# Optimization experiments

Measured on AMD Instinct MI355X. Metric: run time of the kernel, lower is better.

Reference implementation:

```python
import jax, jax.numpy as jnp
import numpy as np

N, L, D = 8192, 50, 64          # batch nodes, history length, embed_dim
NUM_ITEMS, NUM_ATTRS, NUM_FAM = 50000, 100000, 100000


def setup_inputs() -> dict:
    key = jax.random.key(0)
    ks = jax.random.split(key, 12)
    scale = 0.05
    return {
        "nodes": jax.random.randint(ks[0], (N,), 0, NUM_ITEMS),
        "history_va": jax.random.randint(ks[1], (N, L), 0, NUM_ATTRS),
        "history_af": jax.random.randint(ks[2], (N, L), 0, NUM_FAM),
        "v2e_w": jax.random.normal(ks[3], (NUM_ITEMS, D), jnp.float32) * scale,
        "a2e_w": jax.random.normal(ks[4], (NUM_ATTRS, D), jnp.float32) * scale,
        "f2e_w": jax.random.normal(ks[5], (NUM_FAM, D), jnp.float32) * scale,
        "W1": jax.random.normal(ks[6], (3 * D, D), jnp.float32) * scale,
        "b1": jnp.zeros((D,), jnp.float32),
        "W2": jax.random.normal(ks[7], (D, D), jnp.float32) * scale,
        "b2": jnp.zeros((D,), jnp.float32),
        "w3": jax.random.normal(ks[8], (D, 1), jnp.float32) * scale,
        "b3": jnp.zeros((1,), jnp.float32),
    }


def reference(nodes, history_va, history_af, v2e_w, a2e_w, f2e_w,
              W1, b1, W2, b2, w3, b3):
    # Batched form of the per-node loop (va=True branch).
    e_va = a2e_w[history_va]                       # [N, L, D] gathered attr embeds
    e_af = f2e_w[history_af]                       # [N, L, D] gathered famous embeds
    va_rep = v2e_w[nodes]                          # [N, D]    target item embed
    rep = jnp.broadcast_to(va_rep[:, None, :], e_va.shape)
    x = jnp.concatenate([e_va, rep, e_af], axis=-1)  # [N, L, 3D]
    h = jax.nn.relu(x @ W1 + b1)                   # [N, L, D]
    h = jax.nn.relu(h @ W2 + b2)                   # [N, L, D]
    scores = (h @ w3 + b3)[..., 0]                 # [N, L]
    att = jax.nn.softmax(scores, axis=1)           # softmax over history dim
    # e_va.T @ att per node  ==  weighted sum over history
    return jnp.einsum("nld,nl->nd", e_va, att)     # [N, D]
```

## Files before the change

### kernel.cpp

```cpp
#include <hip/hip_runtime.h>
#include <hip/hip_bf16.h>

typedef __bf16    bf16x8 __attribute__((ext_vector_type(8)));
typedef __bf16    bf16x4 __attribute__((ext_vector_type(4)));
typedef _Float16  f16x8  __attribute__((ext_vector_type(8)));
typedef _Float16  f16x4  __attribute__((ext_vector_type(4)));
typedef float     f32x4  __attribute__((ext_vector_type(4)));

#define HL 50
#define DD 64


__global__ __launch_bounds__(256, 4) void prep_all_kernel(
    const int*   __restrict__ nodes,
    const float* __restrict__ v2e,
    const float* __restrict__ a2e,
    const float* __restrict__ f2e,
    const float* __restrict__ W1,
    const float* __restrict__ b1,
    const float* __restrict__ W2,
    const float* __restrict__ b2,
    const float* __restrict__ w3,
    _Float16* __restrict__ A2, _Float16* __restrict__ F2,
    _Float16* __restrict__ E16, _Float16* __restrict__ ba16,
    _Float16* __restrict__ w2f, float* __restrict__ wsc,
    int nA, int nF, int N, int GA, int GF, int GB)
{
    __shared__ __align__(16) _Float16 es[64 * 72];
    const int tid  = threadIdx.x;
    const int w    = tid >> 6, lane = tid & 63;
    const int lq   = lane & 15, quad = lane >> 4;
    const int col  = w * 16 + lq;
    const int bid  = blockIdx.x;

    if (bid < GA + GF) {
        const bool  isA   = (bid < GA);
        const int   rb    = isA ? bid : bid - GA;
        const int   nrows = isA ? nA : nF;
        const float* src  = isA ? a2e : f2e;
        const float* Wp   = isA ? W1 : (W1 + 128 * DD);
        _Float16*   dst   = isA ? A2 : F2;
        const int   r0    = rb * 64;

        #pragma unroll
        for (int i = 0; i < 4; ++i) {
            int t = i * 256 + tid;
            int row = t >> 4, q = t & 15;
            int gr = r0 + row; if (gr >= nrows) gr = nrows - 1;
            float4 v = *(const float4*)(src + (size_t)gr * DD + q * 4);
            f16x4 pk = {(_Float16)v.x, (_Float16)v.y, (_Float16)v.z, (_Float16)v.w};
            *(f16x4*)&es[row * 72 + q * 4] = pk;
            if (isA) *(f16x4*)(E16 + (size_t)gr * DD + q * 4) = pk;
        }
        f16x8 bfr[2];
        #pragma unroll
        for (int t = 0; t < 2; ++t)
            #pragma unroll
            for (int j = 0; j < 8; ++j)
                bfr[t][j] = (_Float16)Wp[(t * 32 + quad * 8 + j) * DD + col];
        __syncthreads();

        f32x4 acc[4];
        #pragma unroll
        for (int mt = 0; mt < 4; ++mt) acc[mt] = (f32x4){0.f, 0.f, 0.f, 0.f};
        #pragma unroll
        for (int t = 0; t < 2; ++t)
            #pragma unroll
            for (int mt = 0; mt < 4; ++mt) {
                f16x8 a = *(const f16x8*)&es[(mt * 16 + lq) * 72 + t * 32 + quad * 8];
                acc[mt] = __builtin_amdgcn_mfma_f32_16x16x32_f16(a, bfr[t], acc[mt], 0, 0, 0);
            }
        __syncthreads();
        #pragma unroll
        for (int mt = 0; mt < 4; ++mt)
            #pragma unroll
            for (int r = 0; r < 4; ++r)
                es[(mt * 16 + quad * 4 + r) * 72 + col] = (_Float16)acc[mt][r];
        __syncthreads();
        {
            #pragma unroll
            for (int h = 0; h < 2; ++h) {
                int t   = h * 256 + tid;
                int row = t >> 3, seg = t & 7;
                int gr  = r0 + row;
                if (gr < nrows) {
                    f16x8 vv = *(const f16x8*)&es[row * 72 + seg * 8];
                    *(f16x8*)(dst + (size_t)gr * DD + seg * 8) = vv;
                }
            }
        }
    } else if (bid < GA + GF + GB) {
        const int n0 = (bid - GA - GF) * 64;
        #pragma unroll
        for (int i = 0; i < 4; ++i) {
            int t = i * 256 + tid;
            int row = t >> 4, q = t & 15;
            int gn = n0 + row; if (gn >= N) gn = N - 1;
            int idx = nodes[gn];
            float4 v = *(const float4*)(v2e + (size_t)idx * DD + q * 4);
            f16x4 pk = {(_Float16)v.x, (_Float16)v.y, (_Float16)v.z, (_Float16)v.w};
            *(f16x4*)&es[row * 72 + q * 4] = pk;
        }
        f16x8 bfr[2];
        #pragma unroll
        for (int t = 0; t < 2; ++t)
            #pragma unroll
            for (int j = 0; j < 8; ++j)
                bfr[t][j] = (_Float16)W1[(64 + t * 32 + quad * 8 + j) * DD + col];
        const float b1c = b1[col];
        __syncthreads();

        f32x4 acc[4];
        #pragma unroll
        for (int mt = 0; mt < 4; ++mt) acc[mt] = (f32x4){0.f, 0.f, 0.f, 0.f};
        #pragma unroll
        for (int t = 0; t < 2; ++t)
            #pragma unroll
            for (int mt = 0; mt < 4; ++mt) {
                f16x8 a = *(const f16x8*)&es[(mt * 16 + lq) * 72 + t * 32 + quad * 8];
                acc[mt] = __builtin_amdgcn_mfma_f32_16x16x32_f16(a, bfr[t], acc[mt], 0, 0, 0);
            }
        #pragma unroll
        for (int mt = 0; mt < 4; ++mt)
            #pragma unroll
            for (int r = 0; r < 4; ++r) {
                int gn = n0 + mt * 16 + quad * 4 + r;
                if (gn < N) ba16[(size_t)gn * DD + col] = (_Float16)(acc[mt][r] + b1c);
            }
    } else {
        const int ln = tid & 63, c0 = tid >> 6;
        #pragma unroll
        for (int h = 0; h < 2; ++h) {
            int combo = c0 + 4 * h;
            int ct = combo >> 1, t = combo & 1;
            _Float16* d = w2f + ((size_t)combo * 64 + ln) * 8;
            #pragma unroll
            for (int j = 0; j < 8; ++j)
                d[j] = (_Float16)W2[(t * 32 + (ln >> 4) * 8 + j) * DD + ct * 16 + (ln & 15)];
        }
        if (tid < 64) { wsc[tid] = w3[tid]; wsc[64 + tid] = b2[tid]; }
    }
}

__global__ __launch_bounds__(256, 4) void va_main_kernel(
    const int*      __restrict__ hva,
    const int*      __restrict__ haf,
    const _Float16* __restrict__ A2,
    const _Float16* __restrict__ F2,
    const _Float16* __restrict__ E16,
    const _Float16* __restrict__ ba16,
    const _Float16* __restrict__ w2f,
    const float*    __restrict__ wsc,
    float*          __restrict__ out, int Ntot)
{
    const int tid  = threadIdx.x;
    const int w    = tid >> 6;
    const int lane = tid & 63;
    const int lq   = lane & 15;
    const int quad = lane >> 4;
    const int node = blockIdx.x * 4 + w;
    if (node >= Ntot) return;

    const int* hb = hva + node * HL;
    const int* fb = haf + node * HL;
    const int lclamp = (lane < HL) ? lane : 0;
    const int iv  = hb[lclamp];
    const int ifv = fb[lclamp];

    f16x8 bag[2];
    #pragma unroll
    for (int t = 0; t < 2; ++t)
        bag[t] = *(const f16x8*)(ba16 + (size_t)node * DD + t * 32 + quad * 8);

    f16x8 a2g[4][2], f2g[4][2];
    #pragma unroll
    for (int mt = 0; mt < 4; ++mt) {
        const int row = mt * 16 + lq;
        const int ia  = __shfl(iv,  row);
        const int ifm = __shfl(ifv, row);
        const bool valid = (row < HL);
        #pragma unroll
        for (int t = 0; t < 2; ++t) {
            if (valid) {
                a2g[mt][t] = *(const f16x8*)(A2 + (size_t)ia  * DD + t * 32 + quad * 8);
                f2g[mt][t] = *(const f16x8*)(F2 + (size_t)ifm * DD + t * 32 + quad * 8);
            }
        }
    }

    f16x8 h1f[4][2];
    #pragma unroll
    for (int mt = 0; mt < 4; ++mt) {
        const bool valid = (mt * 16 + lq) < HL;
        #pragma unroll
        for (int t = 0; t < 2; ++t) {
            f16x8 h = a2g[mt][t] + f2g[mt][t] + bag[t];
            #pragma unroll
            for (int j = 0; j < 8; ++j)
                h1f[mt][t][j] = (valid && h[j] > (_Float16)0.f) ? h[j] : (_Float16)0.f;
        }
    }

    float sc[4][4];
    #pragma unroll
    for (int mt = 0; mt < 4; ++mt)
        #pragma unroll
        for (int r = 0; r < 4; ++r) sc[mt][r] = 0.f;

    #pragma unroll
    for (int ct = 0; ct < 4; ++ct) {
        const float b2c = wsc[64 + ct * 16 + lq];
        const float w3c = wsc[ct * 16 + lq];
        f16x8 bfr[2];
        #pragma unroll
        for (int t = 0; t < 2; ++t)
            bfr[t] = *(const f16x8*)(w2f + ((size_t)(ct * 2 + t) * 64 + lane) * 8);
        #pragma unroll
        for (int mt = 0; mt < 4; ++mt) {
            f32x4 acc = {b2c, b2c, b2c, b2c};
            #pragma unroll
            for (int t = 0; t < 2; ++t)
                acc = __builtin_amdgcn_mfma_f32_16x16x32_f16(h1f[mt][t], bfr[t], acc, 0, 0, 0);
            #pragma unroll
            for (int r = 0; r < 4; ++r)
                sc[mt][r] = fmaf(fmaxf(acc[r], 0.f), w3c, sc[mt][r]);
        }
    }

    #pragma unroll
    for (int mt = 0; mt < 4; ++mt)
        #pragma unroll
        for (int r = 0; r < 4; ++r)
            #pragma unroll
            for (int m = 1; m < 16; m <<= 1)
                sc[mt][r] += __shfl_xor(sc[mt][r], m);

    #pragma unroll
    for (int r = 0; r < 4; ++r)
        if (48 + quad * 4 + r >= HL) sc[3][r] = -3.0e38f;

    float mx = sc[0][0];
    #pragma unroll
    for (int mt = 0; mt < 4; ++mt)
        #pragma unroll
        for (int r = 0; r < 4; ++r) mx = fmaxf(mx, sc[mt][r]);
    mx = fmaxf(mx, __shfl_xor(mx, 16));
    mx = fmaxf(mx, __shfl_xor(mx, 32));

    float sm = 0.f;
    #pragma unroll
    for (int mt = 0; mt < 4; ++mt)
        #pragma unroll
        for (int r = 0; r < 4; ++r) {
            sc[mt][r] = __expf(sc[mt][r] - mx);
            sm += sc[mt][r];
        }
    sm += __shfl_xor(sm, 16);
    sm += __shfl_xor(sm, 32);
    const float inv = 1.f / sm;

    float oa[4] = {0.f, 0.f, 0.f, 0.f};
    #pragma unroll
    for (int l = 0; l < HL; ++l) {
        const int   srcl = ((l >> 2) & 3) << 4;
        const float av   = __shfl(sc[l >> 4][l & 3], srcl);
        const int   idx  = __builtin_amdgcn_readlane(iv, l);
        oa[l & 3] = fmaf(av, (float)E16[(size_t)idx * DD + lane], oa[l & 3]);
    }
    out[(size_t)node * DD + lane] = ((oa[0] + oa[1]) + (oa[2] + oa[3])) * inv;
}

#define FMR  112
#define FMT  7
#define FXSS 136

__global__ __launch_bounds__(256) void fb_prep_kernel(
    const float* __restrict__ W1, const float* __restrict__ W2,
    const float* __restrict__ w3, const float* __restrict__ b1,
    const float* __restrict__ b2,
    __bf16* __restrict__ wf, float* __restrict__ wsc)
{
    const int tid  = threadIdx.x;
    const int quad = tid >> 6;
    const int col  = tid & 63;
    __bf16* dst = wf + tid * 64;
    #pragma unroll
    for (int t = 0; t < 4; ++t)
        #pragma unroll
        for (int j = 0; j < 8; ++j) {
            int keff = t * 32 + quad * 8 + j;
            int krow = (keff < 64) ? keff : keff + 64;
            dst[t * 8 + j] = (__bf16)W1[krow * 64 + col];
        }
    #pragma unroll
    for (int t = 0; t < 2; ++t)
        #pragma unroll
        for (int j = 0; j < 8; ++j) {
            dst[32 + t * 8 + j] = (__bf16)W1[(64 + t * 32 + quad * 8 + j) * 64 + col];
            dst[48 + t * 8 + j] = (__bf16)W2[(t * 32 + quad * 8 + j) * 64 + col];
        }
    if (tid < 64) {
        wsc[tid] = w3[tid]; wsc[64 + tid] = b1[tid]; wsc[128 + tid] = b2[tid];
    }
}

__global__ __launch_bounds__(256, 5) void fb_agg_kernel(
    const int* __restrict__ nodes, const int* __restrict__ hva,
    const int* __restrict__ haf, const float* __restrict__ v2e,
    const float* __restrict__ a2e, const float* __restrict__ f2e,
    const __bf16* __restrict__ wf, const float* __restrict__ wsc,
    float* __restrict__ out)
{
    __shared__ __bf16 xs[FMR * FXSS];
    __shared__ float  pbuf[4 * FMR];
    const int tid = threadIdx.x;
    const int w = tid >> 6, lane = tid & 63, lq = lane & 15, quad = lane >> 4;
    const int col = w * 16 + lq;
    const int n0 = blockIdx.x * 2;
    {
        const int* hb = hva + n0 * HL;
        const int* fb = haf + n0 * HL;
        #pragma unroll
        for (int i = 0; i < 13; ++i) {
            int t = i * 256 + tid;
            if (t < 2 * HL * 2 * 16) {
                int r = t >> 4, q = t & 15;
                bool va = (r < 2 * HL);
                int gr = va ? r : r - 2 * HL;
                int idx = va ? hb[gr] : fb[gr];
                const float* src = (va ? a2e : f2e) + (size_t)idx * DD + q * 4;
                float4 v = *(const float4*)src;
                bf16x4 pk = {(__bf16)v.x, (__bf16)v.y, (__bf16)v.z, (__bf16)v.w};
                *(bf16x4*)&xs[gr * FXSS + (va ? 0 : DD) + q * 4] = pk;
            }
        }
    }
    bf16x8 repf[2];
    #pragma unroll
    for (int t = 0; t < 2; ++t)
        #pragma unroll
        for (int j = 0; j < 8; ++j) repf[t][j] = (__bf16)0.f;
    if (lq < 2) {
        int nd = nodes[n0 + lq];
        const float* rp = v2e + (size_t)nd * DD;
        #pragma unroll
        for (int t = 0; t < 2; ++t) {
            float4 v0 = *(const float4*)(rp + t * 32 + quad * 8);
            float4 v1 = *(const float4*)(rp + t * 32 + quad * 8 + 4);
            repf[t] = (bf16x8){(__bf16)v0.x, (__bf16)v0.y, (__bf16)v0.z, (__bf16)v0.w,
                               (__bf16)v1.x, (__bf16)v1.y, (__bf16)v1.z, (__bf16)v1.w};
        }
    }
    const __bf16* fbp = wf + (size_t)(quad * 64 + col) * 64;
    bf16x8 b1f[4], b1u[2], b2f[2];
    #pragma unroll
    for (int t = 0; t < 4; ++t) b1f[t] = *(const bf16x8*)(fbp + t * 8);
    #pragma unroll
    for (int t = 0; t < 2; ++t) {
        b1u[t] = *(const bf16x8*)(fbp + 32 + t * 8);
        b2f[t] = *(const bf16x8*)(fbp + 48 + t * 8);
    }
    const float w3c = wsc[col];
    const float b1c = wsc[64 + col];
    const float b2c = wsc[128 + col];
    f32x4 rb = {0.f, 0.f, 0.f, 0.f};
    #pragma unroll
    for (int t = 0; t < 2; ++t)
        rb = __builtin_amdgcn_mfma_f32_16x16x32_bf16(repf[t], b1u[t], rb, 0, 0, 0);
    const float bias0 = __shfl(rb[0], lq) + b1c;
    const float bias1 = __shfl(rb[1], lq) + b1c;
    __syncthreads();
    f32x4 acc[FMT];
    #pragma unroll
    for (int mt = 0; mt < FMT; ++mt)
        #pragma unroll
        for (int r = 0; r < 4; ++r) {
            int gr = mt * 16 + quad * 4 + r;
            acc[mt][r] = (gr >= HL) ? bias1 : bias0;
        }
    #pragma unroll
    for (int t = 0; t < 4; ++t)
        #pragma unroll
        for (int mt = 0; mt < FMT; ++mt) {
            bf16x8 a = *(const bf16x8*)&xs[(mt * 16 + lq) * FXSS + t * 32 + quad * 8];
            acc[mt] = __builtin_amdgcn_mfma_f32_16x16x32_bf16(a, b1f[t], acc[mt], 0, 0, 0);
        }
    __syncthreads();
    #pragma unroll
    for (int mt = 0; mt < FMT; ++mt)
        #pragma unroll
        for (int r = 0; r < 4; ++r) {
            int gr = mt * 16 + quad * 4 + r;
            xs[gr * FXSS + DD + col] = (__bf16)fmaxf(acc[mt][r], 0.f);
        }
    __syncthreads();
    f32x4 a2[FMT];
    #pragma unroll
    for (int mt = 0; mt < FMT; ++mt) a2[mt] = (f32x4){b2c, b2c, b2c, b2c};
    #pragma unroll
    for (int t = 0; t < 2; ++t)
        #pragma unroll
        for (int mt = 0; mt < FMT; ++mt) {
            bf16x8 a = *(const bf16x8*)&xs[(mt * 16 + lq) * FXSS + DD + t * 32 + quad * 8];
            a2[mt] = __builtin_amdgcn_mfma_f32_16x16x32_bf16(a, b2f[t], a2[mt], 0, 0, 0);
        }
    #pragma unroll
    for (int mt = 0; mt < FMT; ++mt) {
        float p0 = fmaxf(a2[mt][0], 0.f) * w3c;
        float p1 = fmaxf(a2[mt][1], 0.f) * w3c;
        float p2 = fmaxf(a2[mt][2], 0.f) * w3c;
        float p3 = fmaxf(a2[mt][3], 0.f) * w3c;
        #pragma unroll
        for (int m = 1; m < 16; m <<= 1) {
            p0 += __shfl_xor(p0, m); p1 += __shfl_xor(p1, m);
            p2 += __shfl_xor(p2, m); p3 += __shfl_xor(p3, m);
        }
        if (lq == 0) {
            int rowb = mt * 16 + quad * 4;
            pbuf[w * FMR + rowb + 0] = p0; pbuf[w * FMR + rowb + 1] = p1;
            pbuf[w * FMR + rowb + 2] = p2; pbuf[w * FMR + rowb + 3] = p3;
        }
    }
    __syncthreads();
    const int n = w & 1, lh = w >> 1;
    float att;
    {
        float s = -3.0e38f;
        if (lane < HL) {
            int gr = n * HL + lane;
            s = pbuf[gr] + pbuf[FMR + gr] + pbuf[2 * FMR + gr] + pbuf[3 * FMR + gr];
        }
        float mx = s;
        #pragma unroll
        for (int m = 1; m < 64; m <<= 1) mx = fmaxf(mx, __shfl_xor(mx, m));
        float e = (lane < HL) ? __expf(s - mx) : 0.f;
        float sm = e;
        #pragma unroll
        for (int m = 1; m < 64; m <<= 1) sm += __shfl_xor(sm, m);
        att = e / sm;
    }
    {
        float o = 0.f;
        const int lb = lh * 25;
        #pragma unroll
        for (int i = 0; i < 25; ++i) {
            int l = lb + i;
            float av = __shfl(att, l);
            o = fmaf(av, (float)xs[(n * HL + l) * FXSS + lane], o);
        }
        float* op = (float*)&xs[(100 + w) * FXSS + DD];
        op[lane] = o;
    }
    __syncthreads();
    if (w < 2) {
        const float* p0 = (const float*)&xs[(100 + w) * FXSS + DD];
        const float* p1 = (const float*)&xs[(100 + w + 2) * FXSS + DD];
        out[(size_t)(n0 + w) * DD + lane] = p0[lane] + p1[lane];
    }
}

extern "C" void kernel_launch(void* const* d_in, const int* in_sizes, int n_in,
                              void* d_out, int out_size, void* d_ws, size_t ws_size,
                              hipStream_t stream) {
    const int*   nodes = (const int*)d_in[0];
    const int*   hva   = (const int*)d_in[1];
    const int*   haf   = (const int*)d_in[2];
    const float* v2e   = (const float*)d_in[3];
    const float* a2e   = (const float*)d_in[4];
    const float* f2e   = (const float*)d_in[5];
    const float* W1    = (const float*)d_in[6];
    const float* b1    = (const float*)d_in[7];
    const float* W2    = (const float*)d_in[8];
    const float* b2    = (const float*)d_in[9];
    const float* w3    = (const float*)d_in[10];
    float* out = (float*)d_out;

    const int N  = in_sizes[0];
    const int nA = in_sizes[4] / DD;
    const int nF = in_sizes[5] / DD;

    size_t offA2 = 0;
    size_t offF2 = (offA2 + (size_t)nA * DD * 2 + 255) & ~(size_t)255;
    size_t offE  = (offF2 + (size_t)nF * DD * 2 + 255) & ~(size_t)255;
    size_t offBA = (offE  + (size_t)nA * DD * 2 + 255) & ~(size_t)255;
    size_t offWF = (offBA + (size_t)N * DD * 2 + 255) & ~(size_t)255;
    size_t offSC = offWF + 8 * 64 * 8 * 2;
    size_t need  = offSC + 128 * 4;

    if (ws_size >= need) {
        _Float16* A2  = (_Float16*)((char*)d_ws + offA2);
        _Float16* F2  = (_Float16*)((char*)d_ws + offF2);
        _Float16* E16 = (_Float16*)((char*)d_ws + offE);
        _Float16* ba  = (_Float16*)((char*)d_ws + offBA);
        _Float16* w2f = (_Float16*)((char*)d_ws + offWF);
        float*    wsc = (float*)((char*)d_ws + offSC);

        const int GA = (nA + 63) / 64;
        const int GF = (nF + 63) / 64;
        const int GB = (N + 63) / 64;
        prep_all_kernel<<<GA + GF + GB + 1, 256, 0, stream>>>(
            nodes, v2e, a2e, f2e, W1, b1, W2, b2, w3,
            A2, F2, E16, ba, w2f, wsc, nA, nF, N, GA, GF, GB);
        va_main_kernel<<<(N + 3) / 4, 256, 0, stream>>>(
            hva, haf, A2, F2, E16, ba, w2f, wsc, out, N);
    } else {
        __bf16* wf  = (__bf16*)d_ws;
        float*  wsc = (float*)((char*)d_ws + 256 * 64 * 2);
        fb_prep_kernel<<<1, 256, 0, stream>>>(W1, W2, w3, b1, b2, wf, wsc);
        fb_agg_kernel<<<N / 2, 256, 0, stream>>>(nodes, hva, haf, v2e, a2e, f2e,
                                                 wf, wsc, out);
    }
}
```

Measured before the change: 149.4 us.

## Restage prep GEMM per-wave with shared weight tile and prefetch history embeds early

In the prep kernel, each wave now owns a 16-row slice and computes all 64 output columns from a weight tile staged once in shared memory. This removes two block-wide barriers, and the global loads of the input rows are issued before the weight conversion. In the main kernel, the 50 E16 history-embedding gathers for the final weighted sum are hoisted to before the MLP. Their latency can then overlap the MFMA and softmax work instead of stalling inside the last loop. The cost is higher register pressure (25 packed half2 values per lane) and more shared memory in the prep kernel, which may reduce occupancy.

```diff
diff --git a/kernel.cpp b/kernel.cpp
--- a/kernel.cpp
+++ b/kernel.cpp
@@ -5,6 +5,7 @@
 typedef __bf16    bf16x4 __attribute__((ext_vector_type(4)));
 typedef _Float16  f16x8  __attribute__((ext_vector_type(8)));
 typedef _Float16  f16x4  __attribute__((ext_vector_type(4)));
+typedef _Float16  f16x2  __attribute__((ext_vector_type(2)));
 typedef float     f32x4  __attribute__((ext_vector_type(4)));
 
 #define HL 50
@@ -26,11 +27,11 @@
     _Float16* __restrict__ w2f, float* __restrict__ wsc,
     int nA, int nF, int N, int GA, int GF, int GB)
 {
+    __shared__ __align__(16) _Float16 wlds[8 * 512];
     __shared__ __align__(16) _Float16 es[64 * 72];
     const int tid  = threadIdx.x;
     const int w    = tid >> 6, lane = tid & 63;
     const int lq   = lane & 15, quad = lane >> 4;
-    const int col  = w * 16 + lq;
     const int bid  = blockIdx.x;
 
     if (bid < GA + GF) {
@@ -40,56 +41,75 @@
         const float* src  = isA ? a2e : f2e;
         const float* Wp   = isA ? W1 : (W1 + 128 * DD);
         _Float16*   dst   = isA ? A2 : F2;
-        const int   r0    = rb * 64;
-
+        const int   r0w   = rb * 64 + w * 16;
+        _Float16*   ws_   = &es[w * 16 * 72];
+
+        float4 v[4];
+        int    grv[4];
         #pragma unroll
         for (int i = 0; i < 4; ++i) {
-            int t = i * 256 + tid;
-            int row = t >> 4, q = t & 15;
-            int gr = r0 + row; if (gr >= nrows) gr = nrows - 1;
-            float4 v = *(const float4*)(src + (size_t)gr * DD + q * 4);
-            f16x4 pk = {(_Float16)v.x, (_Float16)v.y, (_Float16)v.z, (_Float16)v.w};
-            *(f16x4*)&es[row * 72 + q * 4] = pk;
-            if (isA) *(f16x4*)(E16 + (size_t)gr * DD + q * 4) = pk;
-        }
-        f16x8 bfr[2];
+            int t = i * 64 + lane;
+            int row = t >> 4, chunk = t & 15;
+            int gr = r0w + row; if (gr >= nrows) gr = nrows - 1;
+            grv[i] = gr;
+            v[i] = *(const float4*)(src + (size_t)gr * DD + chunk * 4);
+        }
+
+        #pragma unroll
+        for (int h = 0; h < 2; ++h) {
+            int combo = w + 4 * h;
+            int ct = combo >> 1, t = combo & 1;
+            f16x8 pk;
+            #pragma unroll
+            for (int j = 0; j < 8; ++j)
+                pk[j] = (_Float16)Wp[(t * 32 + quad * 8 + j) * DD + ct * 16 + lq];
+            *(f16x8*)&wlds[(size_t)combo * 512 + lane * 8] = pk;
+        }
+
+        #pragma unroll
+        for (int i = 0; i < 4; ++i) {
+            int t = i * 64 + lane;
+            int row = t >> 4, chunk = t & 15;
+            f16x4 pk = {(_Float16)v[i].x, (_Float16)v[i].y,
+                        (_Float16)v[i].z, (_Float16)v[i].w};
+            *(f16x4*)&ws_[row * 72 + chunk * 4] = pk;
+            if (isA) *(f16x4*)(E16 + (size_t)grv[i] * DD + chunk * 4) = pk;
+        }
+
+        __syncthreads();
+
+        f16x8 afr[2];
         #pragma unroll
         for (int t = 0; t < 2; ++t)
-            #pragma unroll
-            for (int j = 0; j < 8; ++j)
-                bfr[t][j] = (_Float16)Wp[(t * 32 + quad * 8 + j) * DD + col];
-        __syncthreads();
-
+            afr[t] = *(const f16x8*)&ws_[lq * 72 + t * 32 + quad * 8];
         f32x4 acc[4];
         #pragma unroll
-        for (int mt = 0; mt < 4; ++mt) acc[mt] = (f32x4){0.f, 0.f, 0.f, 0.f};
-        #pragma unroll
-        for (int t = 0; t < 2; ++t)
-            #pragma unroll
-            for (int mt = 0; mt < 4; ++mt) {
-                f16x8 a = *(const f16x8*)&es[(mt * 16 + lq) * 72 + t * 32 + quad * 8];
-                acc[mt] = __builtin_amdgcn_mfma_f32_16x16x32_f16(a, bfr[t], acc[mt], 0, 0, 0);
+        for (int ct = 0; ct < 4; ++ct) {
+            acc[ct] = (f32x4){0.f, 0.f, 0.f, 0.f};
+            #pragma unroll
+            for (int t = 0; t < 2; ++t) {
+                f16x8 bfr = *(const f16x8*)&wlds[(size_t)(ct * 2 + t) * 512 + lane * 8];
+                acc[ct] = __builtin_amdgcn_mfma_f32_16x16x32_f16(afr[t], bfr, acc[ct], 0, 0, 0);
             }
-        __syncthreads();
-        #pragma unroll
-        for (int mt = 0; mt < 4; ++mt)
+        }
+
+        #pragma unroll
+        for (int ct = 0; ct < 4; ++ct)
             #pragma unroll
             for (int r = 0; r < 4; ++r)
-                es[(mt * 16 + quad * 4 + r) * 72 + col] = (_Float16)acc[mt][r];
-        __syncthreads();
+                ws_[(quad * 4 + r) * 72 + ct * 16 + lq] = (_Float16)acc[ct][r];
         {
-            #pragma unroll
-            for (int h = 0; h < 2; ++h) {
-                int t   = h * 256 + tid;
-                int row = t >> 3, seg = t & 7;
-                int gr  = r0 + row;
-                if (gr < nrows) {
-                    f16x8 vv = *(const f16x8*)&es[row * 72 + seg * 8];
-                    *(f16x8*)(dst + (size_t)gr * DD + seg * 8) = vv;
-                }
+            int row = lane >> 2, g = lane & 3;
+            int gr  = r0w + row;
+            if (gr < nrows) {
+                f16x8 v0 = *(const f16x8*)&ws_[row * 72 + g * 16];
+                f16x8 v1 = *(const f16x8*)&ws_[row * 72 + g * 16 + 8];
+                *(f16x8*)(dst + (size_t)gr * DD + g * 16)     = v0;
+                *(f16x8*)(dst + (size_t)gr * DD + g * 16 + 8) = v1;
             }
         }
     } else if (bid < GA + GF + GB) {
+        const int col = w * 16 + lq;
         const int n0 = (bid - GA - GF) * 64;
         #pragma unroll
         for (int i = 0; i < 4; ++i) {
@@ -188,6 +208,15 @@
         }
     }
 
+    f16x2 ev[25];
+    #pragma unroll
+    for (int i = 0; i < 25; ++i) {
+        const int i0 = __builtin_amdgcn_readlane(iv, 2 * i);
+        const int i1 = __builtin_amdgcn_readlane(iv, 2 * i + 1);
+        ev[i][0] = E16[(size_t)i0 * DD + lane];
+        ev[i][1] = E16[(size_t)i1 * DD + lane];
+    }
+
     f16x8 h1f[4][2];
     #pragma unroll
     for (int mt = 0; mt < 4; ++mt) {
@@ -264,8 +293,7 @@
     for (int l = 0; l < HL; ++l) {
         const int   srcl = ((l >> 2) & 3) << 4;
         const float av   = __shfl(sc[l >> 4][l & 3], srcl);
-        const int   idx  = __builtin_amdgcn_readlane(iv, l);
-        oa[l & 3] = fmaf(av, (float)E16[(size_t)idx * DD + lane], oa[l & 3]);
+        oa[l & 3] = fmaf(av, (float)ev[l >> 1][l & 1], oa[l & 3]);
     }
     out[(size_t)node * DD + lane] = ((oa[0] + oa[1]) + (oa[2] + oa[3])) * inv;
 }
```

Result: slower. 157.4 us (+5.4%).

## Gather raw fp32 embeddings and compute first MLP layer per node

Applied to the files above, without the earlier changes.

Stops precomputing the first-layer projections (A·W1a, F·W1f) over the entire 100k-row attribute and famous tables. The main kernel now gathers the fp32 rows for each node's history, converts them to fp16 and runs the W1 MFMAs itself, with the node bias as the accumulator init. The hidden layer goes through per-wave shared memory to be re-laid out for the W2 MFMA. This removes a full pass over both tables in the prep kernel and the fp16 copy E16. In exchange the gathers read twice the bytes (fp32), there is more compute per node, and the occupancy hint drops to 2 blocks because of register and LDS pressure.

```diff
diff --git a/kernel.cpp b/kernel.cpp
--- a/kernel.cpp
+++ b/kernel.cpp
@@ -14,83 +14,24 @@
 __global__ __launch_bounds__(256, 4) void prep_all_kernel(
     const int*   __restrict__ nodes,
     const float* __restrict__ v2e,
-    const float* __restrict__ a2e,
-    const float* __restrict__ f2e,
     const float* __restrict__ W1,
     const float* __restrict__ b1,
     const float* __restrict__ W2,
     const float* __restrict__ b2,
     const float* __restrict__ w3,
-    _Float16* __restrict__ A2, _Float16* __restrict__ F2,
-    _Float16* __restrict__ E16, _Float16* __restrict__ ba16,
-    _Float16* __restrict__ w2f, float* __restrict__ wsc,
-    int nA, int nF, int N, int GA, int GF, int GB)
+    _Float16* __restrict__ ba16,
+    _Float16* __restrict__ wf, float* __restrict__ wsc,
+    int N, int GB)
 {
     __shared__ __align__(16) _Float16 es[64 * 72];
     const int tid  = threadIdx.x;
     const int w    = tid >> 6, lane = tid & 63;
     const int lq   = lane & 15, quad = lane >> 4;
-    const int col  = w * 16 + lq;
     const int bid  = blockIdx.x;
 
-    if (bid < GA + GF) {
-        const bool  isA   = (bid < GA);
-        const int   rb    = isA ? bid : bid - GA;
-        const int   nrows = isA ? nA : nF;
-        const float* src  = isA ? a2e : f2e;
-        const float* Wp   = isA ? W1 : (W1 + 128 * DD);
-        _Float16*   dst   = isA ? A2 : F2;
-        const int   r0    = rb * 64;
-
-        #pragma unroll
-        for (int i = 0; i < 4; ++i) {
-            int t = i * 256 + tid;
-            int row = t >> 4, q = t & 15;
-            int gr = r0 + row; if (gr >= nrows) gr = nrows - 1;
-            float4 v = *(const float4*)(src + (size_t)gr * DD + q * 4);
-            f16x4 pk = {(_Float16)v.x, (_Float16)v.y, (_Float16)v.z, (_Float16)v.w};
-            *(f16x4*)&es[row * 72 + q * 4] = pk;
-            if (isA) *(f16x4*)(E16 + (size_t)gr * DD + q * 4) = pk;
-        }
-        f16x8 bfr[2];
-        #pragma unroll
-        for (int t = 0; t < 2; ++t)
-            #pragma unroll
-            for (int j = 0; j < 8; ++j)
-                bfr[t][j] = (_Float16)Wp[(t * 32 + quad * 8 + j) * DD + col];
-        __syncthreads();
-
-        f32x4 acc[4];
-        #pragma unroll
-        for (int mt = 0; mt < 4; ++mt) acc[mt] = (f32x4){0.f, 0.f, 0.f, 0.f};
-        #pragma unroll
-        for (int t = 0; t < 2; ++t)
-            #pragma unroll
-            for (int mt = 0; mt < 4; ++mt) {
-                f16x8 a = *(const f16x8*)&es[(mt * 16 + lq) * 72 + t * 32 + quad * 8];
-                acc[mt] = __builtin_amdgcn_mfma_f32_16x16x32_f16(a, bfr[t], acc[mt], 0, 0, 0);
-            }
-        __syncthreads();
-        #pragma unroll
-        for (int mt = 0; mt < 4; ++mt)
-            #pragma unroll
-            for (int r = 0; r < 4; ++r)
-                es[(mt * 16 + quad * 4 + r) * 72 + col] = (_Float16)acc[mt][r];
-        __syncthreads();
-        {
-            #pragma unroll
-            for (int h = 0; h < 2; ++h) {
-                int t   = h * 256 + tid;
-                int row = t >> 3, seg = t & 7;
-                int gr  = r0 + row;
-                if (gr < nrows) {
-                    f16x8 vv = *(const f16x8*)&es[row * 72 + seg * 8];
-                    *(f16x8*)(dst + (size_t)gr * DD + seg * 8) = vv;
-                }
-            }
-        }
-    } else if (bid < GA + GF + GB) {
-        const int n0 = (bid - GA - GF) * 64;
+    if (bid < GB) {
+        const int col = w * 16 + lq;
+        const int n0 = bid * 64;
         #pragma unroll
         for (int i = 0; i < 4; ++i) {
             int t = i * 256 + tid;
@@ -130,29 +71,33 @@
     } else {
         const int ln = tid & 63, c0 = tid >> 6;
         #pragma unroll
-        for (int h = 0; h < 2; ++h) {
-            int combo = c0 + 4 * h;
-            int ct = combo >> 1, t = combo & 1;
-            _Float16* d = w2f + ((size_t)combo * 64 + ln) * 8;
+        for (int h = 0; h < 6; ++h) {
+            int c = c0 + 4 * h;
+            int part = c >> 3, cc = c & 7;
+            int ct = cc >> 1, t = cc & 1;
+            const float* S = (part == 2) ? W2 : W1;
+            int koff = (part == 1) ? 128 : 0;
+            _Float16* d = wf + ((size_t)c * 64 + ln) * 8;
             #pragma unroll
             for (int j = 0; j < 8; ++j)
-                d[j] = (_Float16)W2[(t * 32 + (ln >> 4) * 8 + j) * DD + ct * 16 + (ln & 15)];
+                d[j] = (_Float16)S[(koff + t * 32 + (ln >> 4) * 8 + j) * DD
+                                   + ct * 16 + (ln & 15)];
         }
         if (tid < 64) { wsc[tid] = w3[tid]; wsc[64 + tid] = b2[tid]; }
     }
 }
 
-__global__ __launch_bounds__(256, 4) void va_main_kernel(
+__global__ __launch_bounds__(256, 2) void va_main_kernel(
     const int*      __restrict__ hva,
     const int*      __restrict__ haf,
-    const _Float16* __restrict__ A2,
-    const _Float16* __restrict__ F2,
-    const _Float16* __restrict__ E16,
+    const float*    __restrict__ a2e,
+    const float*    __restrict__ f2e,
     const _Float16* __restrict__ ba16,
-    const _Float16* __restrict__ w2f,
+    const _Float16* __restrict__ wf,
     const float*    __restrict__ wsc,
     float*          __restrict__ out, int Ntot)
 {
+    __shared__ __align__(16) _Float16 hs[4][64 * 72];
     const int tid  = threadIdx.x;
     const int w    = tid >> 6;
     const int lane = tid & 63;
@@ -160,6 +105,7 @@
     const int quad = lane >> 4;
     const int node = blockIdx.x * 4 + w;
     if (node >= Ntot) return;
+    _Float16* ws_ = hs[w];
 
     const int* hb = hva + node * HL;
     const int* fb = haf + node * HL;
@@ -167,39 +113,94 @@
     const int iv  = hb[lclamp];
     const int ifv = fb[lclamp];
 
-    f16x8 bag[2];
-    #pragma unroll
-    for (int t = 0; t < 2; ++t)
-        bag[t] = *(const f16x8*)(ba16 + (size_t)node * DD + t * 32 + quad * 8);
-
-    f16x8 a2g[4][2], f2g[4][2];
+    float4 ra[4][2][2];
     #pragma unroll
     for (int mt = 0; mt < 4; ++mt) {
         const int row = mt * 16 + lq;
-        const int ia  = __shfl(iv,  row);
+        const int ia  = __shfl(iv, row);
+        #pragma unroll
+        for (int t = 0; t < 2; ++t) {
+            const float* p = a2e + (size_t)ia * DD + t * 32 + quad * 8;
+            ra[mt][t][0] = *(const float4*)p;
+            ra[mt][t][1] = *(const float4*)(p + 4);
+        }
+    }
+    f16x8 xa[4][2];
+    #pragma unroll
+    for (int mt = 0; mt < 4; ++mt)
+        #pragma unroll
+        for (int t = 0; t < 2; ++t) {
+            float4 v0 = ra[mt][t][0], v1 = ra[mt][t][1];
+            xa[mt][t] = (f16x8){(_Float16)v0.x, (_Float16)v0.y, (_Float16)v0.z, (_Float16)v0.w,
+                                (_Float16)v1.x, (_Float16)v1.y, (_Float16)v1.z, (_Float16)v1.w};
+        }
+
+    float4 rf[4][2][2];
+    #pragma unroll
+    for (int mt = 0; mt < 4; ++mt) {
+        const int row = mt * 16 + lq;
         const int ifm = __shfl(ifv, row);
-        const bool valid = (row < HL);
-        #pragma unroll
-        for (int t = 0; t < 2; ++t) {
-            if (valid) {
-                a2g[mt][t] = *(const f16x8*)(A2 + (size_t)ia  * DD + t * 32 + quad * 8);
-                f2g[mt][t] = *(const f16x8*)(F2 + (size_t)ifm * DD + t * 32 + quad * 8);
+        #pragma unroll
+        for (int t = 0; t < 2; ++t) {
+            const float* p = f2e + (size_t)ifm * DD + t * 32 + quad * 8;
+            rf[mt][t][0] = *(const float4*)p;
+            rf[mt][t][1] = *(const float4*)(p + 4);
+        }
+    }
+
+    f32x4 acc[4][4];
+    #pragma unroll
+    for (int ct = 0; ct < 4; ++ct) {
+        const float bav = (float)ba16[(size_t)node * DD + ct * 16 + lq];
+        #pragma unroll
+        for (int mt = 0; mt < 4; ++mt)
+            acc[mt][ct] = (f32x4){bav, bav, bav, bav};
+    }
+    #pragma unroll
+    for (int ct = 0; ct < 4; ++ct)
+        #pragma unroll
+        for (int t = 0; t < 2; ++t) {
+            f16x8 bfr = *(const f16x8*)(wf + ((size_t)(ct * 2 + t) * 64 + lane) * 8);
+            #pragma unroll
+            for (int mt = 0; mt < 4; ++mt)
+                acc[mt][ct] = __builtin_amdgcn_mfma_f32_16x16x32_f16(xa[mt][t], bfr, acc[mt][ct], 0, 0, 0);
+        }
+    f16x8 xf[4][2];
+    #pragma unroll
+    for (int mt = 0; mt < 4; ++mt)
+        #pragma unroll
+        for (int t = 0; t < 2; ++t) {
+            float4 v0 = rf[mt][t][0], v1 = rf[mt][t][1];
+            xf[mt][t] = (f16x8){(_Float16)v0.x, (_Float16)v0.y, (_Float16)v0.z, (_Float16)v0.w,
+                                (_Float16)v1.x, (_Float16)v1.y, (_Float16)v1.z, (_Float16)v1.w};
+        }
+    #pragma unroll
+    for (int ct = 0; ct < 4; ++ct)
+        #pragma unroll
+        for (int t = 0; t < 2; ++t) {
+            f16x8 bfr = *(const f16x8*)(wf + ((size_t)(8 + ct * 2 + t) * 64 + lane) * 8);
+            #pragma unroll
+            for (int mt = 0; mt < 4; ++mt)
+                acc[mt][ct] = __builtin_amdgcn_mfma_f32_16x16x32_f16(xf[mt][t], bfr, acc[mt][ct], 0, 0, 0);
+        }
+
+    #pragma unroll
+    for (int mt = 0; mt < 4; ++mt)
+        #pragma unroll
+        for (int ct = 0; ct < 4; ++ct)
+            #pragma unroll
+            for (int r = 0; r < 4; ++r) {
+                const int row = mt * 16 + quad * 4 + r;
+                float hv = (row < HL) ? fmaxf(acc[mt][ct][r], 0.f) : 0.f;
+                ws_[row * 72 + ct * 16 + lq] = (_Float16)hv;
             }
-        }
-    }
 
     f16x8 h1f[4][2];
     #pragma unroll
-    for (int mt = 0; mt < 4; ++mt) {
-        const bool valid = (mt * 16 + lq) < HL;
-        #pragma unroll
-        for (int t = 0; t < 2; ++t) {
-            f16x8 h = a2g[mt][t] + f2g[mt][t] + bag[t];
-            #pragma unroll
-            for (int j = 0; j < 8; ++j)
-                h1f[mt][t][j] = (valid && h[j] > (_Float16)0.f) ? h[j] : (_Float16)0.f;
-        }
-    }
+    for (int mt = 0; mt < 4; ++mt)
+        #pragma unroll
+        for (int t = 0; t < 2; ++t)
+            h1f[mt][t] = *(const f16x8*)&ws_[(mt * 16 + lq) * 72 + t * 32 + quad * 8];
 
     float sc[4][4];
     #pragma unroll
@@ -214,16 +215,16 @@
         f16x8 bfr[2];
         #pragma unroll
         for (int t = 0; t < 2; ++t)
-            bfr[t] = *(const f16x8*)(w2f + ((size_t)(ct * 2 + t) * 64 + lane) * 8);
+            bfr[t] = *(const f16x8*)(wf + ((size_t)(16 + ct * 2 + t) * 64 + lane) * 8);
         #pragma unroll
         for (int mt = 0; mt < 4; ++mt) {
-            f32x4 acc = {b2c, b2c, b2c, b2c};
+            f32x4 a2 = {b2c, b2c, b2c, b2c};
             #pragma unroll
             for (int t = 0; t < 2; ++t)
-                acc = __builtin_amdgcn_mfma_f32_16x16x32_f16(h1f[mt][t], bfr[t], acc, 0, 0, 0);
+                a2 = __builtin_amdgcn_mfma_f32_16x16x32_f16(h1f[mt][t], bfr[t], a2, 0, 0, 0);
             #pragma unroll
             for (int r = 0; r < 4; ++r)
-                sc[mt][r] = fmaf(fmaxf(acc[r], 0.f), w3c, sc[mt][r]);
+                sc[mt][r] = fmaf(fmaxf(a2[r], 0.f), w3c, sc[mt][r]);
         }
     }
 
@@ -265,7 +266,7 @@
         const int   srcl = ((l >> 2) & 3) << 4;
         const float av   = __shfl(sc[l >> 4][l & 3], srcl);
         const int   idx  = __builtin_amdgcn_readlane(iv, l);
-        oa[l & 3] = fmaf(av, (float)E16[(size_t)idx * DD + lane], oa[l & 3]);
+        oa[l & 3] = fmaf(av, a2e[(size_t)idx * DD + lane], oa[l & 3]);
     }
     out[(size_t)node * DD + lane] = ((oa[0] + oa[1]) + (oa[2] + oa[3])) * inv;
 }
@@ -476,33 +477,22 @@
     float* out = (float*)d_out;
 
     const int N  = in_sizes[0];
-    const int nA = in_sizes[4] / DD;
-    const int nF = in_sizes[5] / DD;
-
-    size_t offA2 = 0;
-    size_t offF2 = (offA2 + (size_t)nA * DD * 2 + 255) & ~(size_t)255;
-    size_t offE  = (offF2 + (size_t)nF * DD * 2 + 255) & ~(size_t)255;
-    size_t offBA = (offE  + (size_t)nA * DD * 2 + 255) & ~(size_t)255;
+
+    size_t offBA = 0;
     size_t offWF = (offBA + (size_t)N * DD * 2 + 255) & ~(size_t)255;
-    size_t offSC = offWF + 8 * 64 * 8 * 2;
+    size_t offSC = offWF + 24 * 64 * 8 * 2;
     size_t need  = offSC + 128 * 4;
 
     if (ws_size >= need) {
-        _Float16* A2  = (_Float16*)((char*)d_ws + offA2);
-        _Float16* F2  = (_Float16*)((char*)d_ws + offF2);
-        _Float16* E16 = (_Float16*)((char*)d_ws + offE);
         _Float16* ba  = (_Float16*)((char*)d_ws + offBA);
-        _Float16* w2f = (_Float16*)((char*)d_ws + offWF);
+        _Float16* wfr = (_Float16*)((char*)d_ws + offWF);
         float*    wsc = (float*)((char*)d_ws + offSC);
 
-        const int GA = (nA + 63) / 64;
-        const int GF = (nF + 63) / 64;
         const int GB = (N + 63) / 64;
-        prep_all_kernel<<<GA + GF + GB + 1, 256, 0, stream>>>(
-            nodes, v2e, a2e, f2e, W1, b1, W2, b2, w3,
-            A2, F2, E16, ba, w2f, wsc, nA, nF, N, GA, GF, GB);
+        prep_all_kernel<<<GB + 1, 256, 0, stream>>>(
+            nodes, v2e, W1, b1, W2, b2, w3, ba, wfr, wsc, N, GB);
         va_main_kernel<<<(N + 3) / 4, 256, 0, stream>>>(
-            hva, haf, A2, F2, E16, ba, w2f, wsc, out, N);
+            hva, haf, a2e, f2e, ba, wfr, wsc, out, N);
     } else {
         __bf16* wf  = (__bf16*)d_ws;
         float*  wsc = (float*)((char*)d_ws + 256 * 64 * 2);
```

After: 164.7 us. 10.2% more time.
